# Performance work log

Hardware: AMD Instinct MI355X
Metric: run time of the kernel (lower is better)

## Reference

```python
import jax, jax.numpy as jnp
import numpy as np

B, C, H, W = 16, 8, 512, 512
EPS_TH = 1e-14

def setup_inputs() -> dict:
    key = jax.random.key(0)
    x = jax.random.normal(key, (B, C, H, W), dtype=jnp.float32)
    alpha = jnp.full((1,), 0.95, dtype=jnp.float32)
    beta = jnp.full((1,), 8.0, dtype=jnp.float32)
    return {"x": x, "alpha": alpha, "beta": beta}

def reference(x, alpha, beta):
    b, c, h, w = x.shape
    x2 = x.reshape(b * c, h * w)
    # torch.nanquantile with default linear interpolation == jnp.nanquantile
    i1 = jnp.nanquantile(x2, 0.01, axis=1, keepdims=True)   # [B*C, 1]
    i99 = jnp.nanquantile(x2, 0.99, axis=1, keepdims=True)  # [B*C, 1]
    th = (i1 + (i99 - i1) * alpha).reshape(b, c, 1, 1)      # broadcast instead of tile
    mask = (th > EPS_TH).astype(x.dtype)
    th_new = th * mask + (1.0 - mask)
    gate = 1.0 / (1.0 + jnp.exp(-(beta / th_new * (jnp.abs(x) - th * mask))))
    return jax.nn.relu(x) * gate
```

## Files before the change

kernel.cpp:

```cpp
#include <hip/hip_runtime.h>


#define ROWS 128
#define NPR  262144
#define BINS 8192
#define SHIFT 19
#define CAP  4096
#define CBUF 2048

#define K_LO 2621u
#define K_HI 259521u

#define OFF_GH   0
#define OFF_GCNT (ROWS*2*BINS)
#define OFF_SB   (OFF_GCNT + 256)
#define OFF_CAND (OFF_SB + ROWS*8)
#define OFF_QV   (OFF_CAND + ROWS*2*CAP)

typedef float  f32x4 __attribute__((ext_vector_type(4)));

__device__ __forceinline__ unsigned keyOf(float f) {
    unsigned u = __float_as_uint(f);
    return (u & 0x80000000u) ? ~u : (u | 0x80000000u);
}
__device__ __forceinline__ float keyToFloat(unsigned k) {
    unsigned u = (k & 0x80000000u) ? (k & 0x7fffffffu) : ~k;
    return __uint_as_float(u);
}

__global__ __launch_bounds__(1024) void k_hist(const float* __restrict__ x,
                                               unsigned* __restrict__ gh) {
    __shared__ unsigned lh[2][BINS];
    unsigned* flat = &lh[0][0];
    for (int i = threadIdx.x; i < 2 * BINS; i += 1024) flat[i] = 0;
    __syncthreads();
    unsigned* myh = lh[threadIdx.x >> 9];
    const int row  = blockIdx.x >> 1;
    const int half = blockIdx.x & 1;
    const float4* xr = (const float4*)(x + (size_t)row * NPR + (size_t)half * (NPR / 2));
    const int NV = NPR / 2 / 4;
    for (int i = threadIdx.x; i < NV; i += 1024) {
        float4 v = xr[i];
        atomicAdd(&myh[keyOf(v.x) >> SHIFT], 1u);
        atomicAdd(&myh[keyOf(v.y) >> SHIFT], 1u);
        atomicAdd(&myh[keyOf(v.z) >> SHIFT], 1u);
        atomicAdd(&myh[keyOf(v.w) >> SHIFT], 1u);
    }
    __syncthreads();
    unsigned* h = gh + (size_t)blockIdx.x * BINS;
    for (int i = threadIdx.x; i < BINS; i += 1024) h[i] = lh[0][i] + lh[1][i];
}

__global__ __launch_bounds__(256) void k_scan(const unsigned* __restrict__ gh,
                                              unsigned* __restrict__ sbinfo,
                                              unsigned* __restrict__ gcnt) {
    const int row = blockIdx.x;
    const int tid = threadIdx.x;
    if (tid < 2) gcnt[row * 2 + tid] = 0;
    const unsigned* h0 = gh + (size_t)(row * 2) * BINS;
    const unsigned* h1 = h0 + BINS;
    __shared__ unsigned part[256];
    __shared__ unsigned sb[8];
    const int CH = BINS / 256;
    int base = tid * CH;
    unsigned loc[CH];
    unsigned s = 0;
    #pragma unroll
    for (int i = 0; i < CH; ++i) { loc[i] = h0[base + i] + h1[base + i]; s += loc[i]; }
    part[tid] = s;
    __syncthreads();
    if (tid == 0) {
        unsigned run = 0;
        for (int t = 0; t < 256; ++t) { unsigned tmp = part[t]; part[t] = run; run += tmp; }
    }
    __syncthreads();
    {
        unsigned cum = part[tid];
        const unsigned targets[4] = {K_LO, K_LO + 1u, K_HI, K_HI + 1u};
        #pragma unroll
        for (int i = 0; i < CH; ++i) {
            unsigned c = loc[i];
            if (c) {
                #pragma unroll
                for (int t = 0; t < 4; ++t) {
                    if (targets[t] >= cum && targets[t] < cum + c) {
                        if      (t == 0) { sb[0] = base + i; sb[2] = cum; }
                        else if (t == 1) { sb[1] = base + i; }
                        else if (t == 2) { sb[3] = base + i; sb[5] = cum; }
                        else             { sb[4] = base + i; }
                    }
                }
            }
            cum += c;
        }
    }
    __syncthreads();
    if (tid == 0) {
        unsigned* r = sbinfo + row * 8;
        r[0] = sb[0] << SHIFT;
        r[1] = ((sb[1] + 1u) << SHIFT) - 1u;
        r[2] = sb[2];
        r[3] = sb[3] << SHIFT;
        r[4] = ((sb[4] + 1u) << SHIFT) - 1u;
        r[5] = sb[5];
    }
}

__global__ __launch_bounds__(256) void k_collect(const float* __restrict__ x,
                                                 const unsigned* __restrict__ sbinfo,
                                                 unsigned* __restrict__ gcnt,
                                                 unsigned* __restrict__ candg) {
    __shared__ unsigned buf0[CBUF], buf1[CBUF];
    __shared__ unsigned lc[2];
    __shared__ unsigned gbase[2];
    const int row = blockIdx.x >> 4;
    const int blk = blockIdx.x & 15;
    if (threadIdx.x < 2) lc[threadIdx.x] = 0;
    __syncthreads();
    const unsigned* r = sbinfo + row * 8;
    const unsigned klo0 = r[0], khi0 = r[1], klo1 = r[3], khi1 = r[4];
    const float4* xr = (const float4*)(x + (size_t)row * NPR + (size_t)blk * (NPR / 16));
    const int NV = NPR / 16 / 4;
    for (int i = threadIdx.x; i < NV; i += 256) {
        float4 v = xr[i];
        float vv[4] = {v.x, v.y, v.z, v.w};
        #pragma unroll
        for (int j = 0; j < 4; ++j) {
            unsigned key = keyOf(vv[j]);
            if (key >= klo0 && key <= khi0) {
                unsigned p = atomicAdd(&lc[0], 1u);
                if (p < CBUF) buf0[p] = key;
            }
            if (key >= klo1 && key <= khi1) {
                unsigned p = atomicAdd(&lc[1], 1u);
                if (p < CBUF) buf1[p] = key;
            }
        }
    }
    __syncthreads();
    if (threadIdx.x < 2) {
        unsigned n = lc[threadIdx.x]; if (n > CBUF) n = CBUF;
        gbase[threadIdx.x] = atomicAdd(&gcnt[row * 2 + threadIdx.x], n);
    }
    __syncthreads();
    unsigned n0 = lc[0] > CBUF ? CBUF : lc[0];
    unsigned n1 = lc[1] > CBUF ? CBUF : lc[1];
    unsigned* c0 = candg + (size_t)(row * 2) * CAP;
    unsigned* c1 = c0 + CAP;
    for (unsigned i = threadIdx.x; i < n0; i += 256) {
        unsigned p = gbase[0] + i; if (p < CAP) c0[p] = buf0[i];
    }
    for (unsigned i = threadIdx.x; i < n1; i += 256) {
        unsigned p = gbase[1] + i; if (p < CAP) c1[p] = buf1[i];
    }
}

__global__ __launch_bounds__(256) void k_select(const unsigned* __restrict__ candg,
                                                const unsigned* __restrict__ gcnt,
                                                const unsigned* __restrict__ sbinfo,
                                                float* __restrict__ qv) {
    const int rq  = blockIdx.x;
    const int row = rq >> 1;
    const int iq  = rq & 1;
    const int tid = threadIdx.x;
    __shared__ unsigned keys[CAP];
    __shared__ unsigned sh[256];
    __shared__ unsigned svar[4];
    unsigned m = gcnt[rq]; if (m > CAP) m = CAP;
    const unsigned* cand = candg + (size_t)rq * CAP;
    for (unsigned i = tid; i < m; i += 256) keys[i] = cand[i];
    __syncthreads();

    const unsigned cb   = sbinfo[row * 8 + (iq ? 5 : 2)];
    const unsigned t_lo = (iq ? K_HI : K_LO) - cb;
    unsigned prefix = 0, trem = t_lo, cntEq = 0;
    for (int p = 3; p >= 0; --p) {
        sh[tid] = 0;
        __syncthreads();
        for (unsigned i = tid; i < m; i += 256) {
            unsigned key = keys[i];
            bool match = (p == 3) || ((key >> ((p + 1) * 8)) == (prefix >> ((p + 1) * 8)));
            if (match) atomicAdd(&sh[(key >> (p * 8)) & 255u], 1u);
        }
        __syncthreads();
        if (tid == 0) {
            unsigned cum = 0;
            for (int b = 0; b < 256; ++b) {
                unsigned c = sh[b];
                if (trem >= cum && trem < cum + c) { svar[0] = (unsigned)b; svar[1] = cum; svar[2] = c; break; }
                cum += c;
            }
        }
        __syncthreads();
        prefix |= svar[0] << (p * 8);
        trem   -= svar[1];
        cntEq   = svar[2];
        __syncthreads();
    }
    unsigned vlo_key = prefix;
    unsigned cntLess = t_lo - trem;
    unsigned vhi_key;
    if (t_lo + 1u < cntLess + cntEq) {
        vhi_key = vlo_key;
    } else {
        if (tid == 0) svar[3] = 0xFFFFFFFFu;
        __syncthreads();
        for (unsigned i = tid; i < m; i += 256) {
            unsigned key = keys[i];
            if (key > vlo_key) atomicMin(&svar[3], key);
        }
        __syncthreads();
        vhi_key = svar[3];
    }
    if (tid == 0) {
        double frac = iq ? (0.99 * (double)(NPR - 1) - (double)K_HI)
                         : (0.01 * (double)(NPR - 1) - (double)K_LO);
        double vlo = (double)keyToFloat(vlo_key);
        double vhi = (double)keyToFloat(vhi_key);
        qv[rq] = (float)(vlo + (vhi - vlo) * frac);
    }
}

__global__ __launch_bounds__(256) void k_out(const float* __restrict__ x,
                                             const float* __restrict__ alpha,
                                             const float* __restrict__ beta,
                                             const float* __restrict__ qv,
                                             float* __restrict__ out) {
    const int row = blockIdx.x >> 4;
    float q0 = qv[row * 2], q1 = qv[row * 2 + 1];
    float a = alpha[0], bt = beta[0];
    float th = q0 + (q1 - q0) * a;
    bool  msk = th > 1e-14f;
    float thn = msk ? th : 1.0f;
    float thm = msk ? th : 0.0f;
    float nsc = -(bt / thn) * 1.4426950408889634f;
    const float4* xv = (const float4*)x + (size_t)blockIdx.x * 4096;
    f32x4*        ov = (f32x4*)out      + (size_t)blockIdx.x * 4096;
    #pragma unroll 8
    for (int k = 0; k < 16; ++k) {
        int i = k * 256 + threadIdx.x;
        float4 v = xv[i];
        f32x4 o;
        o.x = v.x > 0.f ? v.x * __builtin_amdgcn_rcpf(1.f + __builtin_amdgcn_exp2f(nsc * (fabsf(v.x) - thm))) : 0.f;
        o.y = v.y > 0.f ? v.y * __builtin_amdgcn_rcpf(1.f + __builtin_amdgcn_exp2f(nsc * (fabsf(v.y) - thm))) : 0.f;
        o.z = v.z > 0.f ? v.z * __builtin_amdgcn_rcpf(1.f + __builtin_amdgcn_exp2f(nsc * (fabsf(v.z) - thm))) : 0.f;
        o.w = v.w > 0.f ? v.w * __builtin_amdgcn_rcpf(1.f + __builtin_amdgcn_exp2f(nsc * (fabsf(v.w) - thm))) : 0.f;
        __builtin_nontemporal_store(o, &ov[i]);
    }
}

extern "C" void kernel_launch(void* const* d_in, const int* in_sizes, int n_in,
                              void* d_out, int out_size, void* d_ws, size_t ws_size,
                              hipStream_t stream) {
    const float* x     = (const float*)d_in[0];
    const float* alpha = (const float*)d_in[1];
    const float* beta  = (const float*)d_in[2];
    float* out = (float*)d_out;
    unsigned* ws = (unsigned*)d_ws;
    unsigned* gh     = ws + OFF_GH;
    unsigned* gcnt   = ws + OFF_GCNT;
    unsigned* sbinfo = ws + OFF_SB;
    unsigned* candg  = ws + OFF_CAND;
    float*    qv     = (float*)(ws + OFF_QV);
    k_hist   <<<ROWS * 2,  1024, 0, stream>>>(x, gh);
    k_scan   <<<ROWS,      256,  0, stream>>>(gh, sbinfo, gcnt);
    k_collect<<<ROWS * 16, 256,  0, stream>>>(x, sbinfo, gcnt, candg);
    k_select <<<ROWS * 2,  256,  0, stream>>>(candg, gcnt, sbinfo, qv);
    k_out    <<<ROWS * 16, 256,  0, stream>>>(x, alpha, beta, qv, out);
}
```

Before: 354.7 us.

## Fuse histogram, scan, collect, select and output into one cooperative kernel

Replaces the five separate launches with a single cooperative kernel of 256 blocks of 1024 threads. The stages are separated by grid-wide syncs, and each block reuses one shared buffer across the stages. The aim is to remove per-launch overhead and the idle gaps between dependent kernels, and to keep each block on the same row-half of x through every pass. In exchange, the collect and output stages now run on 256 large blocks instead of 2048 smaller ones. It also adds the cost of the grid barriers and requires every block to be co-resident.

```diff
diff --git a/kernel.cpp b/kernel.cpp
--- a/kernel.cpp
+++ b/kernel.cpp
@@ -1,4 +1,7 @@
 #include <hip/hip_runtime.h>
+#include <hip/hip_cooperative_groups.h>
+
+namespace cg = cooperative_groups;
 
 
 #define ROWS 128
@@ -7,17 +10,19 @@
 #define SHIFT 19
 #define CAP  4096
 #define CBUF 2048
+#define TPB  1024
+#define NBLK 256
 
 #define K_LO 2621u
 #define K_HI 259521u
 
 #define OFF_GH   0
-#define OFF_GCNT (ROWS*2*BINS)
+#define OFF_GCNT (NBLK*BINS)
 #define OFF_SB   (OFF_GCNT + 256)
 #define OFF_CAND (OFF_SB + ROWS*8)
 #define OFF_QV   (OFF_CAND + ROWS*2*CAP)
 
-typedef float  f32x4 __attribute__((ext_vector_type(4)));
+typedef float f32x4 __attribute__((ext_vector_type(4)));
 
 __device__ __forceinline__ unsigned keyOf(float f) {
     unsigned u = __float_as_uint(f);
@@ -28,224 +33,223 @@
     return __uint_as_float(u);
 }
 
-__global__ __launch_bounds__(1024) void k_hist(const float* __restrict__ x,
-                                               unsigned* __restrict__ gh) {
-    __shared__ unsigned lh[2][BINS];
-    unsigned* flat = &lh[0][0];
-    for (int i = threadIdx.x; i < 2 * BINS; i += 1024) flat[i] = 0;
-    __syncthreads();
-    unsigned* myh = lh[threadIdx.x >> 9];
-    const int row  = blockIdx.x >> 1;
-    const int half = blockIdx.x & 1;
+__global__ __launch_bounds__(TPB) void k_fused(const float* __restrict__ x,
+                                               const float* __restrict__ alpha,
+                                               const float* __restrict__ beta,
+                                               unsigned* __restrict__ gh,
+                                               unsigned* __restrict__ sbinfo,
+                                               unsigned* __restrict__ gcnt,
+                                               unsigned* __restrict__ candg,
+                                               float* __restrict__ qv,
+                                               float* __restrict__ out) {
+    cg::grid_group grid = cg::this_grid();
+    __shared__ unsigned smem[2 * BINS];
+    __shared__ unsigned part[256];
+    __shared__ unsigned sb[8];
+    __shared__ unsigned svar[4];
+    __shared__ unsigned lc[2], gbase[2];
+
+    const int bid = blockIdx.x;
+    const int tid = threadIdx.x;
+    const int row  = bid >> 1;
+    const int half = bid & 1;
     const float4* xr = (const float4*)(x + (size_t)row * NPR + (size_t)half * (NPR / 2));
     const int NV = NPR / 2 / 4;
-    for (int i = threadIdx.x; i < NV; i += 1024) {
-        float4 v = xr[i];
-        atomicAdd(&myh[keyOf(v.x) >> SHIFT], 1u);
-        atomicAdd(&myh[keyOf(v.y) >> SHIFT], 1u);
-        atomicAdd(&myh[keyOf(v.z) >> SHIFT], 1u);
-        atomicAdd(&myh[keyOf(v.w) >> SHIFT], 1u);
-    }
+
+    for (int i = tid; i < 2 * BINS; i += TPB) smem[i] = 0;
     __syncthreads();
-    unsigned* h = gh + (size_t)blockIdx.x * BINS;
-    for (int i = threadIdx.x; i < BINS; i += 1024) h[i] = lh[0][i] + lh[1][i];
-}
-
-__global__ __launch_bounds__(256) void k_scan(const unsigned* __restrict__ gh,
-                                              unsigned* __restrict__ sbinfo,
-                                              unsigned* __restrict__ gcnt) {
-    const int row = blockIdx.x;
-    const int tid = threadIdx.x;
-    if (tid < 2) gcnt[row * 2 + tid] = 0;
-    const unsigned* h0 = gh + (size_t)(row * 2) * BINS;
-    const unsigned* h1 = h0 + BINS;
-    __shared__ unsigned part[256];
-    __shared__ unsigned sb[8];
-    const int CH = BINS / 256;
-    int base = tid * CH;
-    unsigned loc[CH];
-    unsigned s = 0;
-    #pragma unroll
-    for (int i = 0; i < CH; ++i) { loc[i] = h0[base + i] + h1[base + i]; s += loc[i]; }
-    part[tid] = s;
+    {
+        unsigned* myh = smem + ((tid >> 9) ? BINS : 0);
+        for (int i = tid; i < NV; i += TPB) {
+            float4 v = xr[i];
+            atomicAdd(&myh[keyOf(v.x) >> SHIFT], 1u);
+            atomicAdd(&myh[keyOf(v.y) >> SHIFT], 1u);
+            atomicAdd(&myh[keyOf(v.z) >> SHIFT], 1u);
+            atomicAdd(&myh[keyOf(v.w) >> SHIFT], 1u);
+        }
+    }
     __syncthreads();
-    if (tid == 0) {
-        unsigned run = 0;
-        for (int t = 0; t < 256; ++t) { unsigned tmp = part[t]; part[t] = run; run += tmp; }
-    }
-    __syncthreads();
-    {
-        unsigned cum = part[tid];
-        const unsigned targets[4] = {K_LO, K_LO + 1u, K_HI, K_HI + 1u};
-        #pragma unroll
-        for (int i = 0; i < CH; ++i) {
-            unsigned c = loc[i];
-            if (c) {
-                #pragma unroll
-                for (int t = 0; t < 4; ++t) {
-                    if (targets[t] >= cum && targets[t] < cum + c) {
-                        if      (t == 0) { sb[0] = base + i; sb[2] = cum; }
-                        else if (t == 1) { sb[1] = base + i; }
-                        else if (t == 2) { sb[3] = base + i; sb[5] = cum; }
-                        else             { sb[4] = base + i; }
+    {
+        unsigned* h = gh + (size_t)bid * BINS;
+        for (int i = tid; i < BINS; i += TPB) h[i] = smem[i] + smem[BINS + i];
+    }
+    grid.sync();
+
+    if (bid < ROWS) {
+        const int CH = BINS / 256;
+        unsigned loc[CH];
+        const int base = (tid & 255) * CH;
+        if (tid < 256) {
+            const unsigned* h0 = gh + (size_t)(bid * 2) * BINS;
+            const unsigned* h1 = h0 + BINS;
+            unsigned s = 0;
+            #pragma unroll
+            for (int i = 0; i < CH; ++i) { loc[i] = h0[base + i] + h1[base + i]; s += loc[i]; }
+            part[tid] = s;
+            if (tid < 2) gcnt[bid * 2 + tid] = 0;
+        }
+        __syncthreads();
+        if (tid == 0) {
+            unsigned run = 0;
+            for (int t = 0; t < 256; ++t) { unsigned tmp = part[t]; part[t] = run; run += tmp; }
+        }
+        __syncthreads();
+        if (tid < 256) {
+            unsigned cum = part[tid];
+            const unsigned targets[4] = {K_LO, K_LO + 1u, K_HI, K_HI + 1u};
+            #pragma unroll
+            for (int i = 0; i < CH; ++i) {
+                unsigned c = loc[i];
+                if (c) {
+                    #pragma unroll
+                    for (int t = 0; t < 4; ++t) {
+                        if (targets[t] >= cum && targets[t] < cum + c) {
+                            if      (t == 0) { sb[0] = base + i; sb[2] = cum; }
+                            else if (t == 1) { sb[1] = base + i; }
+                            else if (t == 2) { sb[3] = base + i; sb[5] = cum; }
+                            else             { sb[4] = base + i; }
+                        }
                     }
                 }
-            }
-            cum += c;
-        }
-    }
-    __syncthreads();
-    if (tid == 0) {
-        unsigned* r = sbinfo + row * 8;
-        r[0] = sb[0] << SHIFT;
-        r[1] = ((sb[1] + 1u) << SHIFT) - 1u;
-        r[2] = sb[2];
-        r[3] = sb[3] << SHIFT;
-        r[4] = ((sb[4] + 1u) << SHIFT) - 1u;
-        r[5] = sb[5];
-    }
-}
-
-__global__ __launch_bounds__(256) void k_collect(const float* __restrict__ x,
-                                                 const unsigned* __restrict__ sbinfo,
-                                                 unsigned* __restrict__ gcnt,
-                                                 unsigned* __restrict__ candg) {
-    __shared__ unsigned buf0[CBUF], buf1[CBUF];
-    __shared__ unsigned lc[2];
-    __shared__ unsigned gbase[2];
-    const int row = blockIdx.x >> 4;
-    const int blk = blockIdx.x & 15;
-    if (threadIdx.x < 2) lc[threadIdx.x] = 0;
-    __syncthreads();
-    const unsigned* r = sbinfo + row * 8;
-    const unsigned klo0 = r[0], khi0 = r[1], klo1 = r[3], khi1 = r[4];
-    const float4* xr = (const float4*)(x + (size_t)row * NPR + (size_t)blk * (NPR / 16));
-    const int NV = NPR / 16 / 4;
-    for (int i = threadIdx.x; i < NV; i += 256) {
-        float4 v = xr[i];
-        float vv[4] = {v.x, v.y, v.z, v.w};
-        #pragma unroll
-        for (int j = 0; j < 4; ++j) {
-            unsigned key = keyOf(vv[j]);
-            if (key >= klo0 && key <= khi0) {
-                unsigned p = atomicAdd(&lc[0], 1u);
-                if (p < CBUF) buf0[p] = key;
-            }
-            if (key >= klo1 && key <= khi1) {
-                unsigned p = atomicAdd(&lc[1], 1u);
-                if (p < CBUF) buf1[p] = key;
-            }
-        }
-    }
-    __syncthreads();
-    if (threadIdx.x < 2) {
-        unsigned n = lc[threadIdx.x]; if (n > CBUF) n = CBUF;
-        gbase[threadIdx.x] = atomicAdd(&gcnt[row * 2 + threadIdx.x], n);
-    }
-    __syncthreads();
-    unsigned n0 = lc[0] > CBUF ? CBUF : lc[0];
-    unsigned n1 = lc[1] > CBUF ? CBUF : lc[1];
-    unsigned* c0 = candg + (size_t)(row * 2) * CAP;
-    unsigned* c1 = c0 + CAP;
-    for (unsigned i = threadIdx.x; i < n0; i += 256) {
-        unsigned p = gbase[0] + i; if (p < CAP) c0[p] = buf0[i];
-    }
-    for (unsigned i = threadIdx.x; i < n1; i += 256) {
-        unsigned p = gbase[1] + i; if (p < CAP) c1[p] = buf1[i];
-    }
-}
-
-__global__ __launch_bounds__(256) void k_select(const unsigned* __restrict__ candg,
-                                                const unsigned* __restrict__ gcnt,
-                                                const unsigned* __restrict__ sbinfo,
-                                                float* __restrict__ qv) {
-    const int rq  = blockIdx.x;
-    const int row = rq >> 1;
-    const int iq  = rq & 1;
-    const int tid = threadIdx.x;
-    __shared__ unsigned keys[CAP];
-    __shared__ unsigned sh[256];
-    __shared__ unsigned svar[4];
-    unsigned m = gcnt[rq]; if (m > CAP) m = CAP;
-    const unsigned* cand = candg + (size_t)rq * CAP;
-    for (unsigned i = tid; i < m; i += 256) keys[i] = cand[i];
-    __syncthreads();
-
-    const unsigned cb   = sbinfo[row * 8 + (iq ? 5 : 2)];
-    const unsigned t_lo = (iq ? K_HI : K_LO) - cb;
-    unsigned prefix = 0, trem = t_lo, cntEq = 0;
-    for (int p = 3; p >= 0; --p) {
-        sh[tid] = 0;
-        __syncthreads();
-        for (unsigned i = tid; i < m; i += 256) {
-            unsigned key = keys[i];
-            bool match = (p == 3) || ((key >> ((p + 1) * 8)) == (prefix >> ((p + 1) * 8)));
-            if (match) atomicAdd(&sh[(key >> (p * 8)) & 255u], 1u);
+                cum += c;
+            }
         }
         __syncthreads();
         if (tid == 0) {
-            unsigned cum = 0;
-            for (int b = 0; b < 256; ++b) {
-                unsigned c = sh[b];
-                if (trem >= cum && trem < cum + c) { svar[0] = (unsigned)b; svar[1] = cum; svar[2] = c; break; }
-                cum += c;
-            }
-        }
-        __syncthreads();
-        prefix |= svar[0] << (p * 8);
-        trem   -= svar[1];
-        cntEq   = svar[2];
-        __syncthreads();
-    }
-    unsigned vlo_key = prefix;
-    unsigned cntLess = t_lo - trem;
-    unsigned vhi_key;
-    if (t_lo + 1u < cntLess + cntEq) {
-        vhi_key = vlo_key;
-    } else {
-        if (tid == 0) svar[3] = 0xFFFFFFFFu;
-        __syncthreads();
-        for (unsigned i = tid; i < m; i += 256) {
-            unsigned key = keys[i];
-            if (key > vlo_key) atomicMin(&svar[3], key);
-        }
-        __syncthreads();
-        vhi_key = svar[3];
-    }
-    if (tid == 0) {
-        double frac = iq ? (0.99 * (double)(NPR - 1) - (double)K_HI)
-                         : (0.01 * (double)(NPR - 1) - (double)K_LO);
-        double vlo = (double)keyToFloat(vlo_key);
-        double vhi = (double)keyToFloat(vhi_key);
-        qv[rq] = (float)(vlo + (vhi - vlo) * frac);
-    }
-}
-
-__global__ __launch_bounds__(256) void k_out(const float* __restrict__ x,
-                                             const float* __restrict__ alpha,
-                                             const float* __restrict__ beta,
-                                             const float* __restrict__ qv,
-                                             float* __restrict__ out) {
-    const int row = blockIdx.x >> 4;
-    float q0 = qv[row * 2], q1 = qv[row * 2 + 1];
-    float a = alpha[0], bt = beta[0];
-    float th = q0 + (q1 - q0) * a;
-    bool  msk = th > 1e-14f;
-    float thn = msk ? th : 1.0f;
-    float thm = msk ? th : 0.0f;
-    float nsc = -(bt / thn) * 1.4426950408889634f;
-    const float4* xv = (const float4*)x + (size_t)blockIdx.x * 4096;
-    f32x4*        ov = (f32x4*)out      + (size_t)blockIdx.x * 4096;
-    #pragma unroll 8
-    for (int k = 0; k < 16; ++k) {
-        int i = k * 256 + threadIdx.x;
-        float4 v = xv[i];
-        f32x4 o;
-        o.x = v.x > 0.f ? v.x * __builtin_amdgcn_rcpf(1.f + __builtin_amdgcn_exp2f(nsc * (fabsf(v.x) - thm))) : 0.f;
-        o.y = v.y > 0.f ? v.y * __builtin_amdgcn_rcpf(1.f + __builtin_amdgcn_exp2f(nsc * (fabsf(v.y) - thm))) : 0.f;
-        o.z = v.z > 0.f ? v.z * __builtin_amdgcn_rcpf(1.f + __builtin_amdgcn_exp2f(nsc * (fabsf(v.z) - thm))) : 0.f;
-        o.w = v.w > 0.f ? v.w * __builtin_amdgcn_rcpf(1.f + __builtin_amdgcn_exp2f(nsc * (fabsf(v.w) - thm))) : 0.f;
-        __builtin_nontemporal_store(o, &ov[i]);
+            unsigned* r = sbinfo + bid * 8;
+            r[0] = sb[0] << SHIFT;
+            r[1] = ((sb[1] + 1u) << SHIFT) - 1u;
+            r[2] = sb[2];
+            r[3] = sb[3] << SHIFT;
+            r[4] = ((sb[4] + 1u) << SHIFT) - 1u;
+            r[5] = sb[5];
+        }
+    }
+    grid.sync();
+
+    {
+        unsigned* buf0 = smem;
+        unsigned* buf1 = smem + CBUF;
+        if (tid < 2) lc[tid] = 0;
+        __syncthreads();
+        const unsigned* r = sbinfo + row * 8;
+        const unsigned klo0 = r[0], khi0 = r[1], klo1 = r[3], khi1 = r[4];
+        for (int i = tid; i < NV; i += TPB) {
+            float4 v = xr[i];
+            float vv[4] = {v.x, v.y, v.z, v.w};
+            #pragma unroll
+            for (int j = 0; j < 4; ++j) {
+                unsigned key = keyOf(vv[j]);
+                if (key >= klo0 && key <= khi0) {
+                    unsigned p = atomicAdd(&lc[0], 1u);
+                    if (p < CBUF) buf0[p] = key;
+                }
+                if (key >= klo1 && key <= khi1) {
+                    unsigned p = atomicAdd(&lc[1], 1u);
+                    if (p < CBUF) buf1[p] = key;
+                }
+            }
+        }
+        __syncthreads();
+        if (tid < 2) {
+            unsigned n = lc[tid]; if (n > CBUF) n = CBUF;
+            gbase[tid] = atomicAdd(&gcnt[row * 2 + tid], n);
+        }
+        __syncthreads();
+        unsigned n0 = lc[0] > CBUF ? CBUF : lc[0];
+        unsigned n1 = lc[1] > CBUF ? CBUF : lc[1];
+        unsigned* c0 = candg + (size_t)(row * 2) * CAP;
+        unsigned* c1 = c0 + CAP;
+        for (unsigned i = tid; i < n0; i += TPB) {
+            unsigned p = gbase[0] + i; if (p < CAP) c0[p] = buf0[i];
+        }
+        for (unsigned i = tid; i < n1; i += TPB) {
+            unsigned p = gbase[1] + i; if (p < CAP) c1[p] = buf1[i];
+        }
+    }
+    grid.sync();
+
+    {
+        const int rq = bid;
+        const int qrow = rq >> 1;
+        const int iq   = rq & 1;
+        unsigned* keys = smem;
+        unsigned* sh   = smem + CAP;
+        unsigned m = gcnt[rq]; if (m > CAP) m = CAP;
+        const unsigned* cand = candg + (size_t)rq * CAP;
+        for (unsigned i = tid; i < m; i += TPB) keys[i] = cand[i];
+        __syncthreads();
+        const unsigned cb   = sbinfo[qrow * 8 + (iq ? 5 : 2)];
+        const unsigned t_lo = (iq ? K_HI : K_LO) - cb;
+        unsigned prefix = 0, trem = t_lo, cntEq = 0;
+        for (int p = 3; p >= 0; --p) {
+            if (tid < 256) sh[tid] = 0;
+            __syncthreads();
+            for (unsigned i = tid; i < m; i += TPB) {
+                unsigned key = keys[i];
+                bool match = (p == 3) || ((key >> ((p + 1) * 8)) == (prefix >> ((p + 1) * 8)));
+                if (match) atomicAdd(&sh[(key >> (p * 8)) & 255u], 1u);
+            }
+            __syncthreads();
+            if (tid == 0) {
+                unsigned cum = 0;
+                for (int b = 0; b < 256; ++b) {
+                    unsigned c = sh[b];
+                    if (trem >= cum && trem < cum + c) { svar[0] = (unsigned)b; svar[1] = cum; svar[2] = c; break; }
+                    cum += c;
+                }
+            }
+            __syncthreads();
+            prefix |= svar[0] << (p * 8);
+            trem   -= svar[1];
+            cntEq   = svar[2];
+            __syncthreads();
+        }
+        unsigned vlo_key = prefix;
+        unsigned cntLess = t_lo - trem;
+        unsigned vhi_key;
+        if (t_lo + 1u < cntLess + cntEq) {
+            vhi_key = vlo_key;
+        } else {
+            if (tid == 0) svar[3] = 0xFFFFFFFFu;
+            __syncthreads();
+            for (unsigned i = tid; i < m; i += TPB) {
+                unsigned key = keys[i];
+                if (key > vlo_key) atomicMin(&svar[3], key);
+            }
+            __syncthreads();
+            vhi_key = svar[3];
+        }
+        if (tid == 0) {
+            double frac = iq ? (0.99 * (double)(NPR - 1) - (double)K_HI)
+                             : (0.01 * (double)(NPR - 1) - (double)K_LO);
+            double vlo = (double)keyToFloat(vlo_key);
+            double vhi = (double)keyToFloat(vhi_key);
+            qv[rq] = (float)(vlo + (vhi - vlo) * frac);
+        }
+    }
+    grid.sync();
+
+    {
+        float q0 = qv[row * 2], q1 = qv[row * 2 + 1];
+        float a = alpha[0], bt = beta[0];
+        float th = q0 + (q1 - q0) * a;
+        bool  msk = th > 1e-14f;
+        float thn = msk ? th : 1.0f;
+        float thm = msk ? th : 0.0f;
+        float nsc = -(bt / thn) * 1.4426950408889634f;
+        f32x4* ov = (f32x4*)(out + (size_t)row * NPR + (size_t)half * (NPR / 2));
+        #pragma unroll 8
+        for (int k = 0; k < 32; ++k) {
+            int i = k * TPB + tid;
+            float4 v = xr[i];
+            f32x4 o;
+            o.x = v.x > 0.f ? v.x * __builtin_amdgcn_rcpf(1.f + __builtin_amdgcn_exp2f(nsc * (fabsf(v.x) - thm))) : 0.f;
+            o.y = v.y > 0.f ? v.y * __builtin_amdgcn_rcpf(1.f + __builtin_amdgcn_exp2f(nsc * (fabsf(v.y) - thm))) : 0.f;
+            o.z = v.z > 0.f ? v.z * __builtin_amdgcn_rcpf(1.f + __builtin_amdgcn_exp2f(nsc * (fabsf(v.z) - thm))) : 0.f;
+            o.w = v.w > 0.f ? v.w * __builtin_amdgcn_rcpf(1.f + __builtin_amdgcn_exp2f(nsc * (fabsf(v.w) - thm))) : 0.f;
+            __builtin_nontemporal_store(o, &ov[i]);
+        }
     }
 }
 
@@ -258,13 +262,11 @@
     float* out = (float*)d_out;
     unsigned* ws = (unsigned*)d_ws;
     unsigned* gh     = ws + OFF_GH;
+    unsigned* sbinfo = ws + OFF_SB;
     unsigned* gcnt   = ws + OFF_GCNT;
-    unsigned* sbinfo = ws + OFF_SB;
     unsigned* candg  = ws + OFF_CAND;
     float*    qv     = (float*)(ws + OFF_QV);
-    k_hist   <<<ROWS * 2,  1024, 0, stream>>>(x, gh);
-    k_scan   <<<ROWS,      256,  0, stream>>>(gh, sbinfo, gcnt);
-    k_collect<<<ROWS * 16, 256,  0, stream>>>(x, sbinfo, gcnt, candg);
-    k_select <<<ROWS * 2,  256,  0, stream>>>(candg, gcnt, sbinfo, qv);
-    k_out    <<<ROWS * 16, 256,  0, stream>>>(x, alpha, beta, qv, out);
-}
+    void* args[] = {(void*)&x, (void*)&alpha, (void*)&beta, (void*)&gh,
+                    (void*)&sbinfo, (void*)&gcnt, (void*)&candg, (void*)&qv, (void*)&out};
+    hipLaunchCooperativeKernel((const void*)k_fused, dim3(NBLK), dim3(TPB), args, 0, stream);
+}
```

Measured after the change: 468.1 us. +32.0%, slower.
